# Kernel tuning notes

Hardware: AMD Instinct MI355X
Metric: run time of the kernel (lower is better)

The kernel has to match this reference:

```python
import jax, jax.numpy as jnp
import numpy as np

HID = 2048; NH = 16; DQN = 128; DR = 64; DV = 128; QLR = 1536; KVLR = 512
DQ = DQN + DR  # 192
S = 2048; B = 2
EPS = 1e-6; BASE = 10000.0


def rmsnorm(x, w, eps=EPS):
    xf = x.astype(jnp.float32)
    v = jnp.mean(jnp.square(xf), axis=-1, keepdims=True)
    return (xf * jax.lax.rsqrt(v + eps)).astype(x.dtype) * w


def rope_cos_sin(seq_len, dim):
    inv_freq = 1.0 / (BASE ** (jnp.arange(0, dim, 2, dtype=jnp.float32) / dim))
    freqs = jnp.outer(jnp.arange(seq_len, dtype=jnp.float32), inv_freq)  # [s, d/2]
    emb = jnp.concatenate([freqs, freqs], axis=-1)  # [s, d]
    return jnp.cos(emb), jnp.sin(emb)


def rotate_half(x):
    x1, x2 = jnp.split(x, 2, axis=-1)
    return jnp.concatenate([-x2, x1], axis=-1)


def apply_rope(q, k, cos, sin, position_ids):
    # DeepSeek-V2 variant: interleaved-pair reorder before rotate_half
    cos = cos[position_ids][:, None]  # [b,1,s,d]
    sin = sin[position_ids][:, None]

    def deinterleave(x):
        b, h, s, d = x.shape
        return x.reshape(b, h, s, d // 2, 2).transpose(0, 1, 2, 4, 3).reshape(b, h, s, d)

    q = deinterleave(q)
    k = deinterleave(k)
    return q * cos + rotate_half(q) * sin, k * cos + rotate_half(k) * sin


def setup_inputs() -> dict:
    key = jax.random.key(0)
    ks = jax.random.split(key, 8)
    hidden_states = jax.random.normal(ks[0], (S, B, HID), dtype=jnp.float32)
    causal = jnp.tril(jnp.ones((S, S), dtype=bool))
    attention_mask = jnp.where(causal, 0.0, -1e9).astype(jnp.float32)
    attention_mask = jnp.broadcast_to(attention_mask[None, None], (B, 1, S, S)) + 0.0
    position_ids = jnp.broadcast_to(jnp.arange(S, dtype=jnp.int64 if jax.config.jax_enable_x64 else jnp.int32), (B, S)) + 0
    w = 0.02
    wq_a = jax.random.normal(ks[1], (QLR, HID), dtype=jnp.float32) * w
    q_a_ln_w = jnp.ones((QLR,), dtype=jnp.float32)
    wq_b = jax.random.normal(ks[2], (NH * DQ, QLR), dtype=jnp.float32) * w
    wkv_a = jax.random.normal(ks[3], (KVLR + DR, HID), dtype=jnp.float32) * w
    kv_a_ln_w = jnp.ones((KVLR,), dtype=jnp.float32)
    wkv_b = jax.random.normal(ks[4], (NH * (DQN + DV), KVLR), dtype=jnp.float32) * w
    wo = jax.random.normal(ks[5], (HID, NH * DV), dtype=jnp.float32) * w
    return {"hidden_states": hidden_states, "attention_mask": attention_mask,
            "position_ids": position_ids, "wq_a": wq_a, "q_a_ln_w": q_a_ln_w,
            "wq_b": wq_b, "wkv_a": wkv_a, "kv_a_ln_w": kv_a_ln_w,
            "wkv_b": wkv_b, "wo": wo}


def reference(hidden_states, attention_mask, position_ids, wq_a, q_a_ln_w, wq_b,
              wkv_a, kv_a_ln_w, wkv_b, wo):
    s, b, _ = hidden_states.shape
    # low-rank Q projection: a -> RMSNorm -> b
    q = hidden_states @ wq_a.T                      # [s,b,QLR]
    q = rmsnorm(q, q_a_ln_w) @ wq_b.T               # [s,b,NH*DQ]
    q = q.reshape(s, b, NH, DQ).transpose(1, 2, 0, 3)  # [b,h,s,dq]
    q_nope, q_pe = q[..., :DQN], q[..., DQN:]
    # joint compressed KV + shared rope key
    ckv = hidden_states @ wkv_a.T                   # [s,b,KVLR+DR]
    compressed_kv, k_pe = ckv[..., :KVLR], ckv[..., KVLR:]
    k_pe = k_pe.reshape(s, b, 1, DR).transpose(1, 2, 0, 3)  # [b,1,s,dr]
    kv = rmsnorm(compressed_kv, kv_a_ln_w) @ wkv_b.T         # [s,b,NH*(DQN+DV)]
    kv = kv.reshape(s, b, NH, DQN + DV).transpose(1, 2, 0, 3)
    k_nope, v = kv[..., :DQN], kv[..., DQN:]
    # partial-dim RoPE
    cos, sin = rope_cos_sin(s, DR)
    q_pe, k_pe = apply_rope(q_pe, k_pe, cos, sin, position_ids)
    query = jnp.concatenate([q_nope, q_pe], axis=-1)                 # [b,h,s,dq]
    key = jnp.concatenate([k_nope, jnp.broadcast_to(k_pe, (b, NH, s, DR))], axis=-1)
    scale = DQ ** -0.5
    scores = jnp.einsum('bhqd,bhkd->bhqk', query, key) * scale + attention_mask
    attn = jax.nn.softmax(scores.astype(jnp.float32), axis=-1).astype(query.dtype)
    out = jnp.einsum('bhqk,bhkd->bhqd', attn, v)    # [b,h,s,dv]
    out = out.transpose(2, 0, 1, 3).reshape(s, b, NH * DV)
    return out @ wo.T                               # [s,b,HID]
```

## Files before the change

kernel.cpp:

```cpp
#include <hip/hip_runtime.h>
#include <cmath>

typedef unsigned short u16;
typedef __bf16 bf16x8 __attribute__((ext_vector_type(8)));
typedef float f32x4 __attribute__((ext_vector_type(4)));

#define MFMA16(a,b,c) __builtin_amdgcn_mfma_f32_16x16x32_bf16((a),(b),(c),0,0,0)

__device__ __forceinline__ u16 f2bf(float f){
  union { float f; unsigned u; } x; x.f = f;
  unsigned r = x.u + 0x7FFFu + ((x.u >> 16) & 1u);
  return (u16)(r >> 16);
}
__device__ __forceinline__ float bf2f(u16 v){
  union { unsigned u; float f; } x; x.u = ((unsigned)v) << 16; return x.f;
}
__device__ __forceinline__ void gload16(const void* g, void* l){
  __builtin_amdgcn_global_load_lds((const __attribute__((address_space(1))) void*)g,
                                   (__attribute__((address_space(3))) void*)l, 16, 0, 0);
}
__device__ __forceinline__ float block_sum256(float v, float* red, int tid){
  #pragma unroll
  for (int off = 32; off; off >>= 1) v += __shfl_xor(v, off);
  if ((tid & 63) == 0) red[tid >> 6] = v;
  __syncthreads();
  return red[0] + red[1] + red[2] + red[3];
}

__global__ __launch_bounds__(256) void k_conv(const float* __restrict__ in,
                                              u16* __restrict__ out, int n4){
  int i = blockIdx.x * 256 + threadIdx.x;
  int stride = gridDim.x * 256;
  for (; i < n4; i += stride){
    float4 v = reinterpret_cast<const float4*>(in)[i];
    ushort4 o; o.x = f2bf(v.x); o.y = f2bf(v.y); o.z = f2bf(v.z); o.w = f2bf(v.w);
    reinterpret_cast<ushort4*>(out)[i] = o;
  }
}

__global__ __launch_bounds__(256) void k_convw(const float* __restrict__ s0,
                                               const float* __restrict__ s1,
                                               const float* __restrict__ s2,
                                               const float* __restrict__ s3,
                                               u16* __restrict__ d0, u16* __restrict__ d1,
                                               u16* __restrict__ d2, u16* __restrict__ d3){
  const int n0 = 1536 * 2048 / 4, n1 = 3072 * 1536 / 4;
  const int n2 = 4096 * 512 / 4,  n3 = 2048 * 2048 / 4;
  const int total = n0 + n1 + n2 + n3;
  const float SCL2 = 0.104117549f;
  int i = blockIdx.x * 256 + threadIdx.x;
  int stride = gridDim.x * 256;
  for (; i < total; i += stride){
    const float* s; u16* d; int j = i; float m = 1.f;
    if (j < n0){ s = s0; d = d0; }
    else if ((j -= n0) < n1){ s = s1; d = d1; m = SCL2; }
    else if ((j -= n1) < n2){ s = s2; d = d2; }
    else { j -= n2; s = s3; d = d3; }
    float4 v = reinterpret_cast<const float4*>(s)[j];
    ushort4 o; o.x = f2bf(v.x * m); o.y = f2bf(v.y * m);
    o.z = f2bf(v.z * m); o.w = f2bf(v.w * m);
    reinterpret_cast<ushort4*>(d)[j] = o;
  }
}

__global__ __launch_bounds__(256) void k_conv_kva(const float* __restrict__ in,
                                                  u16* __restrict__ out){
  const int n4 = 640 * 2048 / 4;
  int i = blockIdx.x * 256 + threadIdx.x;
  int stride = gridDim.x * 256;
  for (; i < n4; i += stride){
    int e = i * 4; int row = e >> 11; int col = e & 2047;
    ushort4 o;
    if (row < 576){
      float4 v = *reinterpret_cast<const float4*>(in + (size_t)row * 2048 + col);
      o.x = f2bf(v.x); o.y = f2bf(v.y); o.z = f2bf(v.z); o.w = f2bf(v.w);
    } else { o.x = 0; o.y = 0; o.z = 0; o.w = 0; }
    reinterpret_cast<ushort4*>(out)[i] = o;
  }
}

template<int OUT_BF16>
__global__ __launch_bounds__(256) void k_gemm(const u16* __restrict__ A,
                                              const u16* __restrict__ Bm,
                                              void* __restrict__ Cv,
                                              int M, int N, int K){
  __shared__ __align__(16) u16 sA[2][128 * 32];
  __shared__ __align__(16) u16 sB[2][128 * 32];
  const int tid = threadIdx.x, w = tid >> 6, l = tid & 63;
  const int ln = l & 15, lg = l >> 4;
  const int id  = blockIdx.x + gridDim.x * blockIdx.y;
  const int nwg = gridDim.x * gridDim.y;
  const int swz = (id & 7) * (nwg >> 3) + (id >> 3);
  const int bx  = swz & (gridDim.x - 1);
  const int by  = swz / gridDim.x;
  const int m0 = bx * 128, n0 = by * 128;
  const int wr = w >> 1, wc = w & 1;
  const int trow = tid >> 2, tcol = (tid & 3) * 8;

  const f32x4 zf = {0.f, 0.f, 0.f, 0.f};
  f32x4 acc[4][4];
  #pragma unroll
  for (int i = 0; i < 4; ++i)
    #pragma unroll
    for (int j = 0; j < 4; ++j) acc[i][j] = zf;

  const u16* ga = A  + (size_t)(m0 + trow) * K + tcol;
  const u16* gb = Bm + (size_t)(n0 + trow) * K + tcol;
  const int nk = K >> 5;

  #define GSTAGE(kt_, bi_) {                                   \
    char* la_ = (char*)sA[bi_] + w * 1024;                     \
    char* lb_ = (char*)sB[bi_] + w * 1024;                     \
    gload16(ga + (kt_) * 32,                  la_);            \
    gload16(ga + (kt_) * 32 + (size_t)64 * K, la_ + 4096);     \
    gload16(gb + (kt_) * 32,                  lb_);            \
    gload16(gb + (kt_) * 32 + (size_t)64 * K, lb_ + 4096);     \
  }

  GSTAGE(0, 0);
  __syncthreads();

  for (int kt = 0; kt < nk; ++kt){
    const int bi = kt & 1;
    if (kt + 1 < nk) GSTAGE(kt + 1, bi ^ 1);

    bf16x8 af[4], bfr[4];
    #pragma unroll
    for (int i = 0; i < 4; ++i)
      af[i] = *(const bf16x8*)&sA[bi][(wr * 64 + i * 16 + ln) * 32 + lg * 8];
    #pragma unroll
    for (int j = 0; j < 4; ++j)
      bfr[j] = *(const bf16x8*)&sB[bi][(wc * 64 + j * 16 + ln) * 32 + lg * 8];
    #pragma unroll
    for (int i = 0; i < 4; ++i)
      #pragma unroll
      for (int j = 0; j < 4; ++j)
        acc[i][j] = MFMA16(af[i], bfr[j], acc[i][j]);

    __syncthreads();
  }
  #undef GSTAGE

  const int mb = m0 + wr * 64, nb = n0 + wc * 64;
  #pragma unroll
  for (int i = 0; i < 4; ++i)
    #pragma unroll
    for (int j = 0; j < 4; ++j)
      #pragma unroll
      for (int r = 0; r < 4; ++r){
        int mm = mb + i * 16 + lg * 4 + r;
        int nn = nb + j * 16 + ln;
        if (OUT_BF16) ((u16*)Cv)[(size_t)mm * N + nn] = f2bf(acc[i][j][r]);
        else          ((float*)Cv)[(size_t)mm * N + nn] = acc[i][j][r];
      }
}

__global__ __launch_bounds__(256) void k_rms_fused(const float* __restrict__ in,
                                                   const float* __restrict__ wq,
                                                   const float* __restrict__ wkv,
                                                   u16* __restrict__ outq,
                                                   u16* __restrict__ outkv,
                                                   u16* __restrict__ kpe){
  __shared__ float red[4];
  const int row = blockIdx.x, tid = threadIdx.x;
  const float* x = in + (size_t)row * 2176;
  float ss = 0.f;
  #pragma unroll
  for (int i = tid; i < 1536; i += 256){ float v = x[i]; ss += v * v; }
  float tot = block_sum256(ss, red, tid);
  float inv = rsqrtf(tot * (1.f / 1536.f) + 1e-6f);
  #pragma unroll
  for (int i = tid; i < 1536; i += 256)
    outq[(size_t)row * 1536 + i] = f2bf(x[i] * inv * wq[i]);
  __syncthreads();
  const float* y = x + 1536;
  float v0 = y[tid], v1 = y[tid + 256];
  float tot2 = block_sum256(v0 * v0 + v1 * v1, red, tid);
  float inv2 = rsqrtf(tot2 * (1.f / 512.f) + 1e-6f);
  outkv[(size_t)row * 512 + tid]       = f2bf(v0 * inv2 * wkv[tid]);
  outkv[(size_t)row * 512 + tid + 256] = f2bf(v1 * inv2 * wkv[tid + 256]);
  if (tid < 32){
    int j = tid;
    float e = y[512 + 2 * j], o = y[512 + 2 * j + 1];
    float pos  = (float)(row >> 1);
    float invf = exp2f(-13.287712379549449f * (float)j * (1.f / 32.f));
    float th = pos * invf, sn = sinf(th), cs = cosf(th);
    kpe[(size_t)row * 64 + j]      = f2bf(e * cs - o * sn);
    kpe[(size_t)row * 64 + 32 + j] = f2bf(o * cs + e * sn);
  }
}

__global__ __launch_bounds__(64) void k_rope_q(const u16* __restrict__ q,
                                               u16* __restrict__ qpe){
  const int sb = blockIdx.x;
  const int h  = blockIdx.y * 2 + (threadIdx.x >> 5);
  const int j  = threadIdx.x & 31;
  const u16* base = q + (size_t)sb * 3072 + h * 192 + 128;
  float e = bf2f(base[2 * j]), o = bf2f(base[2 * j + 1]);
  float pos  = (float)(sb >> 1);
  float invf = exp2f(-13.287712379549449f * (float)j * (1.f / 32.f));
  float th = pos * invf, sn = sinf(th), cs = cosf(th);
  u16* dst = qpe + ((size_t)sb * 16 + h) * 64;
  dst[j]      = f2bf(e * cs - o * sn);
  dst[32 + j] = f2bf(o * cs + e * sn);
}

__global__ __launch_bounds__(256) void k_vtrans(const u16* __restrict__ kv,
                                                u16* __restrict__ vt){
  __shared__ u16 t[64][65];
  const int bh = blockIdx.z, b = bh >> 4, h = bh & 15;
  const int s0 = blockIdx.x * 64, d0 = blockIdx.y * 64;
  const int tid = threadIdx.x;
  #pragma unroll
  for (int i = 0; i < 16; ++i){
    int idx = i * 256 + tid; int si = idx >> 6, di = idx & 63;
    t[si][di] = kv[(size_t)((s0 + si) * 2 + b) * 4096 + h * 256 + 128 + d0 + di];
  }
  __syncthreads();
  #pragma unroll
  for (int i = 0; i < 16; ++i){
    int idx = i * 256 + tid; int di = idx >> 6, si = idx & 63;
    vt[(size_t)((b * 16 + h) * 128 + d0 + di) * 2048 + s0 + si] = t[si][di];
  }
}

__global__ __launch_bounds__(256, 2) void k_attn(const u16* __restrict__ q,
                                                 const u16* __restrict__ qpe,
                                                 const u16* __restrict__ kv,
                                                 const u16* __restrict__ kpe,
                                                 const u16* __restrict__ vt,
                                                 u16* __restrict__ out){
  const int i_ = blockIdx.x + 16 * (blockIdx.y + 16 * blockIdx.z);
  const int j_ = i_ >> 3, x_ = i_ & 7;
  const int g_ = x_ * 4 + (j_ >> 4);
  const int bx = j_ & 15;
  const int h = g_ & 15, b = g_ >> 4;
  const int bh = b * 16 + h;
  const int tid = threadIdx.x, w = tid >> 6, l = tid & 63;
  const int ln = l & 15, lg = l >> 4;

  __shared__ __align__(16) u16 sK[2][64 * 128];
  __shared__ __align__(16) u16 sPE[2][64 * 64];
  __shared__ __align__(16) u16 sV[2][128 * 64];

  const f32x4 zf = {0.f, 0.f, 0.f, 0.f};

  #define PERM(pr_) ((((pr_) >> 5) << 5) + ((((pr_) >> 2) & 3) << 3) + \
                     ((((pr_) >> 4) & 1) << 2) + ((pr_) & 3))
  #define STAGE(kt_, bi_) {                                                     \
    _Pragma("unroll")                                                           \
    for (int p = 0; p < 4; ++p){                                                \
      int o_ = p * 4096 + tid * 16;                                             \
      int pr = o_ >> 8, cl = (o_ >> 4) & 15, cg = cl ^ (pr & 7);                \
      int kl = PERM(pr);                                                        \
      gload16(kv + (size_t)(((kt_) * 64 + kl) * 2 + b) * 4096 + h * 256 + cg * 8, \
              (char*)sK[bi_] + o_);                                             \
    }                                                                           \
    _Pragma("unroll")                                                           \
    for (int p = 0; p < 2; ++p){                                                \
      int o_ = p * 4096 + tid * 16;                                             \
      int pr = o_ >> 7, cl = (o_ >> 4) & 7, cg = cl ^ (pr & 7);                 \
      int kl = PERM(pr);                                                        \
      gload16(kpe + (size_t)(((kt_) * 64 + kl) * 2 + b) * 64 + cg * 8,          \
              (char*)sPE[bi_] + o_);                                            \
    }                                                                           \
    _Pragma("unroll")                                                           \
    for (int p = 0; p < 4; ++p){                                                \
      int o_ = p * 4096 + tid * 16;                                             \
      int row = o_ >> 7, cl = (o_ >> 4) & 7, cg = cl ^ (row & 7);               \
      gload16(vt + (size_t)(bh * 128 + row) * 2048 + (kt_) * 64 + cg * 8,       \
              (char*)sV[bi_] + o_);                                             \
    } }

  for (int half = 0; half < 2; ++half){
    const int qt = half ? (31 - bx) : bx;
    const int qrow0 = qt * 64 + w * 16;
    const int sq = qrow0 + ln;

    bf16x8 qf[6];
    {
      const u16* qr = q + (size_t)(sq * 2 + b) * 3072 + h * 192;
      #pragma unroll
      for (int kb = 0; kb < 4; ++kb) qf[kb] = *(const bf16x8*)(qr + kb * 32 + lg * 8);
      const u16* pr_ = qpe + ((size_t)(sq * 2 + b) * 16 + h) * 64;
      qf[4] = *(const bf16x8*)(pr_ + lg * 8);
      qf[5] = *(const bf16x8*)(pr_ + 32 + lg * 8);
    }

    f32x4 o[8];
    float m_i = -3.0e38f, l_i = 0.f;
    #pragma unroll
    for (int c8 = 0; c8 < 8; ++c8) o[c8] = zf;

    const int nkt = qt + 1;
    STAGE(0, 0);
    __syncthreads();

    for (int kt = 0; kt < nkt; ++kt){
      const int bi = kt & 1;
      if (kt + 1 < nkt) STAGE(kt + 1, bi ^ 1);

      f32x4 s_[4];
      #pragma unroll
      for (int cb = 0; cb < 4; ++cb){
        int rl = cb * 16 + ln, swz = rl & 7;
        bf16x8 kf[6];
        #pragma unroll
        for (int kb = 0; kb < 4; ++kb)
          kf[kb] = *(const bf16x8*)((char*)sK[bi] + rl * 256 + (((kb * 4 + lg) ^ swz) << 4));
        kf[4] = *(const bf16x8*)((char*)sPE[bi] + rl * 128 + ((lg ^ swz) << 4));
        kf[5] = *(const bf16x8*)((char*)sPE[bi] + rl * 128 + (((4 + lg) ^ swz) << 4));
        f32x4 acc = zf;
        #pragma unroll
        for (int kb = 0; kb < 6; ++kb)
          acc = MFMA16(kf[kb], qf[kb], acc);
        s_[cb] = acc;
      }

      const bool needMask = (kt * 64 + 63) > qrow0;
      float mx = -3.0e38f;
      #pragma unroll
      for (int cb = 0; cb < 4; ++cb)
        #pragma unroll
        for (int r = 0; r < 4; ++r){
          float v = s_[cb][r];
          if (needMask){
            int sk = kt * 64 + 32 * (cb >> 1) + 8 * lg + 4 * (cb & 1) + r;
            v = (sk <= sq) ? v : -3.0e38f;
          }
          s_[cb][r] = v;
          mx = fmaxf(mx, v);
        }
      mx = fmaxf(mx, __shfl_xor(mx, 16));
      mx = fmaxf(mx, __shfl_xor(mx, 32));
      if (!__all(mx <= m_i + 11.6f)){
        float mn = fmaxf(m_i, mx);
        float sf = exp2f(m_i - mn);
        m_i = mn;
        l_i *= sf;
        float sf0 = __shfl(sf, 4 * lg + 0);
        float sf1 = __shfl(sf, 4 * lg + 1);
        float sf2 = __shfl(sf, 4 * lg + 2);
        float sf3 = __shfl(sf, 4 * lg + 3);
        #pragma unroll
        for (int c8 = 0; c8 < 8; ++c8){
          o[c8][0] *= sf0; o[c8][1] *= sf1; o[c8][2] *= sf2; o[c8][3] *= sf3;
        }
      }
      float rs = 0.f;
      #pragma unroll
      for (int cb = 0; cb < 4; ++cb)
        #pragma unroll
        for (int r = 0; r < 4; ++r){
          float p = exp2f(s_[cb][r] - m_i);
          s_[cb][r] = p;
          rs += p;
        }
      rs += __shfl_xor(rs, 16);
      rs += __shfl_xor(rs, 32);
      l_i += rs;

      bf16x8 pa[2];
      #pragma unroll
      for (int hf = 0; hf < 2; ++hf){
        unsigned pw0, pw1, pw2, pw3;
        f32x4 sa = s_[hf * 2], sb2 = s_[hf * 2 + 1];
        asm("v_cvt_pk_bf16_f32 %0, %1, %2" : "=v"(pw0) : "v"(sa[0]),  "v"(sa[1]));
        asm("v_cvt_pk_bf16_f32 %0, %1, %2" : "=v"(pw1) : "v"(sa[2]),  "v"(sa[3]));
        asm("v_cvt_pk_bf16_f32 %0, %1, %2" : "=v"(pw2) : "v"(sb2[0]), "v"(sb2[1]));
        asm("v_cvt_pk_bf16_f32 %0, %1, %2" : "=v"(pw3) : "v"(sb2[2]), "v"(sb2[3]));
        union { uint4 u; bf16x8 v; } pk;
        pk.u.x = pw0; pk.u.y = pw1; pk.u.z = pw2; pk.u.w = pw3;
        pa[hf] = pk.v;
      }

      #pragma unroll
      for (int c8 = 0; c8 < 8; ++c8){
        int d = c8 * 16 + ln, swz = d & 7;
        bf16x8 vf0 = *(const bf16x8*)((char*)sV[bi] + d * 128 + ((lg ^ swz) << 4));
        bf16x8 vf1 = *(const bf16x8*)((char*)sV[bi] + d * 128 + (((4 + lg) ^ swz) << 4));
        o[c8] = MFMA16(pa[0], vf0, o[c8]);
        o[c8] = MFMA16(pa[1], vf1, o[c8]);
      }
      __syncthreads();
    }

    float li0 = __shfl(l_i, 4 * lg + 0);
    float li1 = __shfl(l_i, 4 * lg + 1);
    float li2 = __shfl(l_i, 4 * lg + 2);
    float li3 = __shfl(l_i, 4 * lg + 3);
    float iv0 = 1.f / li0, iv1 = 1.f / li1, iv2 = 1.f / li2, iv3 = 1.f / li3;
    int sqr = qrow0 + lg * 4;
    #pragma unroll
    for (int c8 = 0; c8 < 8; ++c8){
      int col = h * 128 + c8 * 16 + ln;
      out[(size_t)((sqr + 0) * 2 + b) * 2048 + col] = f2bf(o[c8][0] * iv0);
      out[(size_t)((sqr + 1) * 2 + b) * 2048 + col] = f2bf(o[c8][1] * iv1);
      out[(size_t)((sqr + 2) * 2 + b) * 2048 + col] = f2bf(o[c8][2] * iv2);
      out[(size_t)((sqr + 3) * 2 + b) * 2048 + col] = f2bf(o[c8][3] * iv3);
    }
  }
  #undef STAGE
  #undef PERM
}

extern "C" void kernel_launch(void* const* d_in, const int* in_sizes, int n_in,
                              void* d_out, int out_size, void* d_ws, size_t ws_size,
                              hipStream_t stream){
  const float* hidden    = (const float*)d_in[0];
  const float* wq_a      = (const float*)d_in[3];
  const float* q_a_ln_w  = (const float*)d_in[4];
  const float* wq_b      = (const float*)d_in[5];
  const float* wkv_a     = (const float*)d_in[6];
  const float* kv_a_ln_w = (const float*)d_in[7];
  const float* wkv_b     = (const float*)d_in[8];
  const float* wo        = (const float*)d_in[9];

  char* ws = (char*)d_ws;
  size_t off = 0;
  auto alloc = [&](size_t bytes){ size_t o = off; off += (bytes + 255) & ~(size_t)255; return o; };
  const size_t SB = 4096;

  u16*   hid_bf   = (u16*)(ws + alloc(SB * 2048 * 2));
  u16*   wqab_bf  = (u16*)(ws + alloc((size_t)2176 * 2048 * 2));
  u16*   wqb_bf   = (u16*)(ws + alloc((size_t)3072 * 1536 * 2));
  u16*   wkvb_bf  = (u16*)(ws + alloc((size_t)4096 * 512 * 2));
  u16*   wo_bf    = (u16*)(ws + alloc((size_t)2048 * 2048 * 2));
  float* qa_f     = (float*)(ws + alloc(SB * 2176 * 4));
  u16*   qrms_bf  = (u16*)(ws + alloc(SB * 1536 * 2));
  u16*   ckvr_bf  = (u16*)(ws + alloc(SB * 512 * 2));
  u16*   kpe_bf   = (u16*)(ws + alloc(SB * 64 * 2));
  u16*   qfull_bf = (u16*)(ws + alloc(SB * 3072 * 2));
  u16*   qpe_bf   = (u16*)(ws + alloc(SB * 16 * 64 * 2));
  u16*   kv_bf    = (u16*)(ws + alloc(SB * 4096 * 2));
  u16*   vt_bf    = hid_bf;
  u16*   attn_bf  = (u16*)qa_f;

  dim3 blk(256);
  k_conv<<<2048, blk, 0, stream>>>(hidden, hid_bf, (int)(SB * 2048 / 4));
  k_convw<<<2048, blk, 0, stream>>>(wq_a, wq_b, wkv_b, wo,
                                    wqab_bf, wqb_bf, wkvb_bf, wo_bf);
  k_conv_kva<<<512, blk, 0, stream>>>(wkv_a, wqab_bf + (size_t)1536 * 2048);
  k_gemm<0><<<dim3(32, 17), blk, 0, stream>>>(hid_bf, wqab_bf, qa_f, 4096, 2176, 2048);
  k_rms_fused<<<4096, blk, 0, stream>>>(qa_f, q_a_ln_w, kv_a_ln_w, qrms_bf, ckvr_bf, kpe_bf);
  k_gemm<1><<<dim3(32, 24), blk, 0, stream>>>(qrms_bf, wqb_bf, qfull_bf, 4096, 3072, 1536);
  k_rope_q<<<dim3(4096, 8), dim3(64), 0, stream>>>(qfull_bf, qpe_bf);
  k_gemm<1><<<dim3(32, 32), blk, 0, stream>>>(ckvr_bf, wkvb_bf, kv_bf, 4096, 4096, 512);
  k_vtrans<<<dim3(32, 2, 32), blk, 0, stream>>>(kv_bf, vt_bf);
  k_attn<<<dim3(16, 16, 2), blk, 0, stream>>>(qfull_bf, qpe_bf, kv_bf, kpe_bf, vt_bf, attn_bf);
  k_gemm<0><<<dim3(32, 16), blk, 0, stream>>>(attn_bf, wo_bf, d_out, 4096, 2048, 2048);
}
```

Baseline: 313.5 us.

## Triple-buffer GEMM LDS pipeline and fuse V transpose into kv GEMM epilogue

The GEMM kernel moves from double to triple LDS buffering. It prefetches two K-tiles ahead and uses explicit vmcnt waits with raw s_barrier in place of a full __syncthreads, so global loads overlap more MFMA work. The kv_b GEMM gets a third epilogue mode that writes the V half directly in transposed layout, which removes the separate k_vtrans kernel and its extra read and write pass. The transposed stores are strided scalar writes, and the extra LDS buffer raises shared-memory use per block.

Result: slower. 323.7 us (+3.3%).

```diff
diff --git a/kernel.cpp b/kernel.cpp
--- a/kernel.cpp
+++ b/kernel.cpp
@@ -79,13 +79,14 @@
   }
 }
 
-template<int OUT_BF16>
+template<int MODE>
 __global__ __launch_bounds__(256) void k_gemm(const u16* __restrict__ A,
                                               const u16* __restrict__ Bm,
                                               void* __restrict__ Cv,
+                                              u16* __restrict__ Vt,
                                               int M, int N, int K){
-  __shared__ __align__(16) u16 sA[2][128 * 32];
-  __shared__ __align__(16) u16 sB[2][128 * 32];
+  __shared__ __align__(16) u16 sA[3][128 * 32];
+  __shared__ __align__(16) u16 sB[3][128 * 32];
   const int tid = threadIdx.x, w = tid >> 6, l = tid & 63;
   const int ln = l & 15, lg = l >> 4;
   const int id  = blockIdx.x + gridDim.x * blockIdx.y;
@@ -118,11 +119,15 @@
   }
 
   GSTAGE(0, 0);
-  __syncthreads();
-
+  GSTAGE(1, 1);
+  asm volatile("s_waitcnt vmcnt(4)" ::: "memory");
+  __builtin_amdgcn_sched_barrier(0);
+  __builtin_amdgcn_s_barrier();
+
+  int bi = 0;
   for (int kt = 0; kt < nk; ++kt){
-    const int bi = kt & 1;
-    if (kt + 1 < nk) GSTAGE(kt + 1, bi ^ 1);
+    int bs = bi + 2; if (bs >= 3) bs -= 3;
+    if (kt + 2 < nk) GSTAGE(kt + 2, bs);
 
     bf16x8 af[4], bfr[4];
     #pragma unroll
@@ -137,7 +142,13 @@
       for (int j = 0; j < 4; ++j)
         acc[i][j] = MFMA16(af[i], bfr[j], acc[i][j]);
 
-    __syncthreads();
+    if (kt + 1 < nk){
+      if (kt + 2 < nk) asm volatile("s_waitcnt vmcnt(4)" ::: "memory");
+      else             asm volatile("s_waitcnt vmcnt(0)" ::: "memory");
+      __builtin_amdgcn_sched_barrier(0);
+      __builtin_amdgcn_s_barrier();
+    }
+    bi = bi + 1; if (bi >= 3) bi = 0;
   }
   #undef GSTAGE
 
@@ -150,8 +161,19 @@
       for (int r = 0; r < 4; ++r){
         int mm = mb + i * 16 + lg * 4 + r;
         int nn = nb + j * 16 + ln;
-        if (OUT_BF16) ((u16*)Cv)[(size_t)mm * N + nn] = f2bf(acc[i][j][r]);
-        else          ((float*)Cv)[(size_t)mm * N + nn] = acc[i][j][r];
+        if (MODE == 0){
+          ((float*)Cv)[(size_t)mm * N + nn] = acc[i][j][r];
+        } else if (MODE == 1){
+          ((u16*)Cv)[(size_t)mm * N + nn] = f2bf(acc[i][j][r]);
+        } else {
+          int c = nn & 255, h = nn >> 8;
+          if (c < 128){
+            ((u16*)Cv)[(size_t)mm * N + nn] = f2bf(acc[i][j][r]);
+          } else {
+            int s = mm >> 1, b = mm & 1, d = c - 128;
+            Vt[((size_t)(b * 16 + h) * 128 + d) * 2048 + s] = f2bf(acc[i][j][r]);
+          }
+        }
       }
 }
 
@@ -205,25 +227,6 @@
   dst[32 + j] = f2bf(o * cs + e * sn);
 }
 
-__global__ __launch_bounds__(256) void k_vtrans(const u16* __restrict__ kv,
-                                                u16* __restrict__ vt){
-  __shared__ u16 t[64][65];
-  const int bh = blockIdx.z, b = bh >> 4, h = bh & 15;
-  const int s0 = blockIdx.x * 64, d0 = blockIdx.y * 64;
-  const int tid = threadIdx.x;
-  #pragma unroll
-  for (int i = 0; i < 16; ++i){
-    int idx = i * 256 + tid; int si = idx >> 6, di = idx & 63;
-    t[si][di] = kv[(size_t)((s0 + si) * 2 + b) * 4096 + h * 256 + 128 + d0 + di];
-  }
-  __syncthreads();
-  #pragma unroll
-  for (int i = 0; i < 16; ++i){
-    int idx = i * 256 + tid; int di = idx >> 6, si = idx & 63;
-    vt[(size_t)((b * 16 + h) * 128 + d0 + di) * 2048 + s0 + si] = t[si][di];
-  }
-}
-
 __global__ __launch_bounds__(256, 2) void k_attn(const u16* __restrict__ q,
                                                  const u16* __restrict__ qpe,
                                                  const u16* __restrict__ kv,
@@ -441,12 +444,11 @@
   k_convw<<<2048, blk, 0, stream>>>(wq_a, wq_b, wkv_b, wo,
                                     wqab_bf, wqb_bf, wkvb_bf, wo_bf);
   k_conv_kva<<<512, blk, 0, stream>>>(wkv_a, wqab_bf + (size_t)1536 * 2048);
-  k_gemm<0><<<dim3(32, 17), blk, 0, stream>>>(hid_bf, wqab_bf, qa_f, 4096, 2176, 2048);
+  k_gemm<0><<<dim3(32, 17), blk, 0, stream>>>(hid_bf, wqab_bf, qa_f, nullptr, 4096, 2176, 2048);
   k_rms_fused<<<4096, blk, 0, stream>>>(qa_f, q_a_ln_w, kv_a_ln_w, qrms_bf, ckvr_bf, kpe_bf);
-  k_gemm<1><<<dim3(32, 24), blk, 0, stream>>>(qrms_bf, wqb_bf, qfull_bf, 4096, 3072, 1536);
+  k_gemm<1><<<dim3(32, 24), blk, 0, stream>>>(qrms_bf, wqb_bf, qfull_bf, nullptr, 4096, 3072, 1536);
   k_rope_q<<<dim3(4096, 8), dim3(64), 0, stream>>>(qfull_bf, qpe_bf);
-  k_gemm<1><<<dim3(32, 32), blk, 0, stream>>>(ckvr_bf, wkvb_bf, kv_bf, 4096, 4096, 512);
-  k_vtrans<<<dim3(32, 2, 32), blk, 0, stream>>>(kv_bf, vt_bf);
+  k_gemm<2><<<dim3(32, 32), blk, 0, stream>>>(ckvr_bf, wkvb_bf, kv_bf, vt_bf, 4096, 4096, 512);
   k_attn<<<dim3(16, 16, 2), blk, 0, stream>>>(qfull_bf, qpe_bf, kv_bf, kpe_bf, vt_bf, attn_bf);
-  k_gemm<0><<<dim3(32, 16), blk, 0, stream>>>(attn_bf, wo_bf, d_out, 4096, 2048, 2048);
-}
+  k_gemm<0><<<dim3(32, 16), blk, 0, stream>>>(attn_bf, wo_bf, d_out, nullptr, 4096, 2048, 2048);
+}
```
